# Optimization experiments

Hardware: AMD Instinct MI355X
Metric: run time of the kernel (lower is better)

The kernel has to match this reference:

```python
import jax, jax.numpy as jnp
import numpy as np

NUM_EMBEDDINGS = 8192
EMBEDDING_DIM = 256
COMMITMENT_COST = 0.25


def setup_inputs() -> dict:
    key = jax.random.key(0)
    k1, k2 = jax.random.split(key)
    z_e = jax.random.normal(k1, (32, EMBEDDING_DIM, 32, 32), dtype=jnp.float32)
    # nn.init.uniform_(weight, -1/K, 1/K)
    bound = 1.0 / NUM_EMBEDDINGS
    emb_w = jax.random.uniform(k2, (NUM_EMBEDDINGS, EMBEDDING_DIM), dtype=jnp.float32,
                               minval=-bound, maxval=bound)
    return {"z_e": z_e, "emb_w": emb_w}


def reference(z_e, emb_w):
    b, c, h, w = z_e.shape
    orig_dtype = z_e.dtype
    z = z_e.astype(jnp.float32)
    emb = emb_w.astype(jnp.float32)
    # [B,C,H,W] -> [N, C]
    z_flat = z.transpose(0, 2, 3, 1).reshape(-1, c)
    distances = (jnp.sum(z_flat * z_flat, axis=1, keepdims=True)
                 - 2.0 * (z_flat @ emb.T)
                 + jnp.sum(emb * emb, axis=1))
    encoding_indices = jnp.argmin(distances, axis=1)  # [N]
    z_q = emb[encoding_indices].reshape(b, h, w, c).transpose(0, 3, 1, 2)
    # eval path: commitment = cc * mse(stop_grad(z_e), z_q); codebook = mse(...)
    mse = jnp.mean((jax.lax.stop_gradient(z) - z_q) ** 2)
    vq_loss = (1.0 + COMMITMENT_COST) * mse
    # straight-through estimator
    z_q_st = (z + jax.lax.stop_gradient(z_q - z)).astype(orig_dtype)
    # perplexity from code usage histogram
    n_tokens = encoding_indices.shape[0]
    counts = jnp.zeros((NUM_EMBEDDINGS,), jnp.float32).at[encoding_indices].add(1.0)
    avg_probs = counts / n_tokens
    perplexity = jnp.exp(-jnp.sum(avg_probs * jnp.log(jnp.clip(avg_probs, 1e-10, None))))
    indices = encoding_indices.reshape(b, h, w)
    return z_q_st, vq_loss, perplexity, indices
```

## Files before the change

kernel.cpp:

```cpp
#include <hip/hip_runtime.h>
#include <hip/hip_fp16.h>
#include <cmath>
#include <float.h>

#define NUM_EMB 8192
#define DIM 256
#define HW 1024
#define N_TOK 32768
#define KSPLIT 2
#define KRANGE (NUM_EMB/KSPLIT)
#define OUT_ZQ_ELEMS 8388608

#define CAP 48
#define MARGIN_GP 0.4f

#define BM 128
#define BCODES 64
#define NBUF (KRANGE/BCODES)

#define WS_MSE    0
#define WS_COUNTS 64
#define WS_CNT    (WS_COUNTS + NUM_EMB*4)
#define WS_MEMSET_END (WS_CNT + KSPLIT*N_TOK*4)
#define WS_Z2     WS_MEMSET_END
#define WS_CANDI  (WS_Z2 + N_TOK*4)

typedef _Float16 half8 __attribute__((ext_vector_type(8)));
typedef _Float16 half4v __attribute__((ext_vector_type(4)));
typedef float f32x16 __attribute__((ext_vector_type(16)));
typedef __attribute__((address_space(3))) void lds_void;
typedef __attribute__((address_space(1))) const void gbl_void;

__global__ __launch_bounds__(256) void vq_pack_z(
    const float* __restrict__ z, _Float16* __restrict__ zh, float* __restrict__ z2)
{
    __shared__ float zt[32][257];
    __shared__ float rr[32][16];
    int t = threadIdx.x;
    int n0 = blockIdx.x * 32;
    int b = n0 >> 10, hw0 = n0 & 1023;
    const float* zb = z + (size_t)b * DIM * HW + hw0;
    int tn = t & 31, tc = t >> 5;
    #pragma unroll 4
    for (int it = 0; it < 32; it++) {
        int c = it * 8 + tc;
        zt[tn][c] = zb[(size_t)c * HW + tn];
    }
    __syncthreads();
    int tn2 = t & 31, tj = t >> 5;
    #pragma unroll
    for (int h = 0; h < 2; h++) {
        float v0 = zt[tn2][h*128 + tj];
        float r = __fmul_rn(v0, v0);
        for (int i = 8; i < 128; i += 8) {
            float v = zt[tn2][h*128 + i + tj];
            r = __fadd_rn(r, __fmul_rn(v, v));
        }
        rr[tn2][h*8 + tj] = r;
    }
    int row = t >> 3, seg = t & 7;
    half8 outv[4];
    #pragma unroll
    for (int q = 0; q < 4; q++)
        #pragma unroll
        for (int u = 0; u < 8; u++)
            outv[q][u] = (_Float16)zt[row][seg*32 + q*8 + u];
    half8* dst = (half8*)(zh + (size_t)(n0 + row) * DIM + seg * 32);
    #pragma unroll
    for (int q = 0; q < 4; q++) dst[q] = outv[q];
    __syncthreads();
    if (t < 32) {
        const float* rw = rr[t];
        float h0 = __fadd_rn(__fadd_rn(__fadd_rn(rw[0], rw[1]), __fadd_rn(rw[2], rw[3])),
                             __fadd_rn(__fadd_rn(rw[4], rw[5]), __fadd_rn(rw[6], rw[7])));
        float h1 = __fadd_rn(__fadd_rn(__fadd_rn(rw[8], rw[9]), __fadd_rn(rw[10], rw[11])),
                             __fadd_rn(__fadd_rn(rw[12], rw[13]), __fadd_rn(rw[14], rw[15])));
        z2[n0 + t] = __fadd_rn(h0, h1);
    }
}

__global__ __launch_bounds__(256) void vq_pack_e(
    const float* __restrict__ emb, _Float16* __restrict__ eh)
{
    int i = blockIdx.x * 256 + threadIdx.x;
    float4 v = ((const float4*)emb)[i];
    half4v h;
    h[0] = (_Float16)(v.x * 8192.0f);
    h[1] = (_Float16)(v.y * 8192.0f);
    h[2] = (_Float16)(v.z * 8192.0f);
    h[3] = (_Float16)(v.w * 8192.0f);
    *(half4v*)(eh + (size_t)i * 4) = h;
}

__global__ __launch_bounds__(512) void vq_dist_kernel(
    const _Float16* __restrict__ zh, const _Float16* __restrict__ eh,
    int* __restrict__ cnt, unsigned short* __restrict__ candi)
{
    __shared__ _Float16 Bs[2][16384];
    __shared__ float mx[2][BM];
    __shared__ int cntL[BM];
    int t = threadIdx.x;
    int w = t >> 6, lane = t & 63;
    int lm = lane & 31, lh = lane >> 5;
    int r = w >> 1, c = w & 1;
    int n0 = blockIdx.x * BM;
    int ks = blockIdx.y;
    int kbase = ks * KRANGE;

    if (t < BM) {
        cntL[t] = 0;
        mx[0][t] = -1e30f;
        mx[1][t] = -1e30f;
    }

    const _Float16* arow = zh + (size_t)(n0 + r*32 + lm) * DIM + lh * 8;
    half8 A[16];
    #pragma unroll
    for (int s = 0; s < 16; s++)
        A[s] = *(const half8*)(arow + s * 16);

    auto STAGE = [&](int ii, int b) {
        int cb0 = kbase + ii * BCODES;
        #pragma unroll
        for (int rr = 0; rr < 4; rr++) {
            int p = rr * 512 + t;
            int cd = p >> 5;
            int oc = ((p & 31) - cd) & 31;
            __builtin_amdgcn_global_load_lds(
                (gbl_void*)(eh + (size_t)(cb0 + cd) * DIM + oc * 8),
                (lds_void*)((char*)&Bs[b][0] + p * 16), 16, 0, 0);
        }
    };

    float m[16];
    #pragma unroll
    for (int e = 0; e < 16; e++) m[e] = -1e30f;

    int cl = c * 32 + lm;

    auto COMPUTE = [&](int i, int b) {
        {
            const float4* mb = (const float4*)&mx[c ^ 1][r * 32 + 4 * lh];
            #pragma unroll
            for (int g = 0; g < 4; g++) {
                float4 v = mb[2 * g];
                m[4*g+0] = fmaxf(m[4*g+0], v.x);
                m[4*g+1] = fmaxf(m[4*g+1], v.y);
                m[4*g+2] = fmaxf(m[4*g+2], v.z);
                m[4*g+3] = fmaxf(m[4*g+3], v.w);
            }
        }

        const _Float16* Bb = &Bs[b][0] + (size_t)cl * 256;
        f32x16 acc;
        #pragma unroll
        for (int e = 0; e < 16; e++) acc[e] = 0.f;

        __builtin_amdgcn_s_setprio(1);
        #pragma unroll
        for (int s = 0; s < 16; s++) {
            half8 bf = *(const half8*)(Bb + (((s*2 + lh) + cl) & 31) * 8);
            acc = __builtin_amdgcn_mfma_f32_32x32x16_f16(A[s], bf, acc, 0, 0, 0);
        }
        __builtin_amdgcn_s_setprio(0);

        #pragma unroll
        for (int e = 0; e < 16; e++) m[e] = fmaxf(m[e], acc[e]);
        bool doRed = (i < 4) || ((i & 3) == 3);
        if (doRed) {
            #pragma unroll
            for (int e = 0; e < 16; e++) {
                float q = m[e];
                #pragma unroll
                for (int o = 1; o <= 16; o <<= 1) q = fmaxf(q, __shfl_xor(q, o));
                m[e] = q;
            }
            if (lm == 0) {
                float4* mb = (float4*)&mx[c][r * 32 + 4 * lh];
                #pragma unroll
                for (int g = 0; g < 4; g++) {
                    float4 v = { m[4*g+0], m[4*g+1], m[4*g+2], m[4*g+3] };
                    mb[2 * g] = v;
                }
            }
        }
        int cb = kbase + i * BCODES;
        #pragma unroll
        for (int e = 0; e < 16; e++) {
            if (acc[e] > m[e] - MARGIN_GP) {
                int rowe = (e & 3) + 8 * (e >> 2) + 4 * lh;
                int tok = r * 32 + rowe;
                int slot = atomicAdd(&cntL[tok], 1);
                if (slot < CAP)
                    candi[((size_t)ks * N_TOK + n0 + tok) * CAP + slot] =
                        (unsigned short)(cb + cl);
            }
        }
    };

    STAGE(0, 0);
    for (int i = 0; i < NBUF; i += 2) {
        __syncthreads();
        STAGE(i + 1, 1);
        COMPUTE(i, 0);
        __syncthreads();
        if (i + 2 < NBUF) STAGE(i + 2, 0);
        COMPUTE(i + 1, 1);
    }

    __syncthreads();
    if (t < BM) cnt[ks * N_TOK + n0 + t] = cntL[t];
}

#define GT 32
__global__ __launch_bounds__(256) void vq_rg_kernel(
    const float* __restrict__ z, const float* __restrict__ emb,
    const float* __restrict__ z2, const int* __restrict__ cnt,
    const unsigned short* __restrict__ candi,
    int* __restrict__ counts, double* __restrict__ mse_sum,
    float* __restrict__ out_zq, float* __restrict__ out_idx)
{
    __shared__ float zs[GT][257];
    __shared__ float zq[GT][DIM];
    __shared__ unsigned long long kmin[GT];
    __shared__ int sidx[GT];
    __shared__ double red[4];
    int t = threadIdx.x;
    int n0 = blockIdx.x * GT;
    int b = n0 >> 10, hw0 = n0 & 1023;
    int lane = t & 63, w = t >> 6;

    {
        int nn = t & 31, cg = t >> 5;
        const float* zb = z + (size_t)b * DIM * HW + hw0 + nn;
        #pragma unroll 4
        for (int i = 0; i < 32; i++) {
            int c = i*8 + cg;
            zs[nn][c] = zb[(size_t)c * HW];
        }
    }
    if (t < GT) kmin[t] = ~0ULL;
    __syncthreads();

    int tcs0[8], po[9];
    int ovf8 = 0;
    po[0] = 0;
    #pragma unroll
    for (int i = 0; i < 8; i++) {
        int n = n0 + w*8 + i;
        int c0 = cnt[n], c1 = cnt[N_TOK + n];
        if (c0 > CAP || c1 > CAP) { c0 = 0; c1 = 0; ovf8 |= (1 << i); }
        tcs0[i] = c0;
        po[i+1] = po[i] + c0 + c1;
    }
    int total = po[8];

    for (int base = 0; base < total; base += 64) {
        int g = base + lane;
        unsigned long long key = ~0ULL;
        int mytok = -1;
        if (g < total) {
            int i = 0;
            #pragma unroll
            for (int q = 1; q < 8; q++) i += (g >= po[q]);
            int sl = g - po[i];
            int n = n0 + w*8 + i;
            int s = sl >= tcs0[i];
            int slot = s ? sl - tcs0[i] : sl;
            int code = candi[((size_t)s * N_TOK + n) * CAP + slot];
            int tok = w*8 + i;
            float accv = 0.f;
            const float4* ep = (const float4*)(emb + (size_t)code * DIM);
            #pragma unroll 8
            for (int q4 = 0; q4 < 64; q4++) {
                float4 e4 = ep[q4];
                accv = fmaf(zs[tok][q4*4+0], e4.x, accv);
                accv = fmaf(zs[tok][q4*4+1], e4.y, accv);
                accv = fmaf(zs[tok][q4*4+2], e4.z, accv);
                accv = fmaf(zs[tok][q4*4+3], e4.w, accv);
            }
            float d = fmaf(-2.f, accv, z2[n]);
            key = ((unsigned long long)__float_as_uint(d) << 32) | (unsigned)code;
            mytok = tok;
        }
        #pragma unroll
        for (int i = 0; i < 8; i++) {
            unsigned long long kk = (mytok == w*8 + i) ? key : ~0ULL;
            #pragma unroll
            for (int o = 32; o > 0; o >>= 1) {
                unsigned long long ob = __shfl_xor(kk, o);
                if (ob < kk) kk = ob;
            }
            if (lane == 0 && kk < kmin[w*8 + i]) kmin[w*8 + i] = kk;
        }
    }

    for (int i = 0; i < 8; i++) if (ovf8 & (1 << i)) {
        int tok = w*8 + i, n = n0 + tok;
        float z2n = z2[n];
        unsigned long long bst = ~0ULL;
        for (int k = lane; k < NUM_EMB; k += 64) {
            float accv = 0.f;
            const float4* ep = (const float4*)(emb + (size_t)k * DIM);
            #pragma unroll 8
            for (int q4 = 0; q4 < 64; q4++) {
                float4 e4 = ep[q4];
                accv = fmaf(zs[tok][q4*4+0], e4.x, accv);
                accv = fmaf(zs[tok][q4*4+1], e4.y, accv);
                accv = fmaf(zs[tok][q4*4+2], e4.z, accv);
                accv = fmaf(zs[tok][q4*4+3], e4.w, accv);
            }
            float d = fmaf(-2.f, accv, z2n);
            unsigned long long kk =
                ((unsigned long long)__float_as_uint(d) << 32) | (unsigned)k;
            if (kk < bst) bst = kk;
        }
        #pragma unroll
        for (int o = 32; o > 0; o >>= 1) {
            unsigned long long ob = __shfl_xor(bst, o);
            if (ob < bst) bst = ob;
        }
        if (lane == 0 && bst < kmin[tok]) kmin[tok] = bst;
    }
    __syncthreads();

    if (t < GT) {
        int bi = (int)(kmin[t] & 0xffffffffu);
        sidx[t] = bi;
        out_idx[n0 + t] = (float)bi;
        atomicAdd(&counts[bi], 1);
    }
    __syncthreads();

    for (int m = w*8; m < w*8 + 8; m++) {
        int row = sidx[m];
        float4 v = *(const float4*)(emb + (size_t)row * DIM + lane * 4);
        int cb = (lane + m) & 63;
        *(float4*)&zq[m][cb * 4] = v;
    }
    __syncthreads();

    int nn = t & 31, cc = t >> 5;
    float* op = out_zq + (size_t)b * DIM * HW + hw0 + nn;
    float lsum = 0.f;
    #pragma unroll 4
    for (int i = 0; i < 32; i++) {
        int c = i*8 + cc;
        int cb = ((c >> 2) + nn) & 63;
        float q = zq[nn][cb*4 + (c & 3)];
        float zv = zs[nn][c];
        op[(size_t)c * HW] = __fadd_rn(zv, __fsub_rn(q, zv));
        float d = zv - q;
        lsum = fmaf(d, d, lsum);
    }
    double ds = (double)lsum;
    #pragma unroll
    for (int off = 32; off > 0; off >>= 1)
        ds += __shfl_down(ds, off);
    if (lane == 0) red[w] = ds;
    __syncthreads();
    if (t == 0) atomicAdd(mse_sum, red[0] + red[1] + red[2] + red[3]);
}

__global__ __launch_bounds__(256) void vq_finalize_kernel(
    const double* __restrict__ mse_sum, const int* __restrict__ counts,
    float* __restrict__ out_scalars)
{
    __shared__ float red[4];
    int t = threadIdx.x;
    float local = 0.f;
    for (int k = t; k < NUM_EMB; k += 256) {
        int c = counts[k];
        if (c > 0) {
            float p = (float)c * (1.0f / (float)N_TOK);
            local += p * logf(p);
        }
    }
    int lane = t & 63, w = t >> 6;
    #pragma unroll
    for (int off = 32; off > 0; off >>= 1)
        local += __shfl_down(local, off);
    if (lane == 0) red[w] = local;
    __syncthreads();
    if (t == 0) {
        float s = red[0] + red[1] + red[2] + red[3];
        out_scalars[0] = 1.25f * (float)(*mse_sum * (1.0 / (double)OUT_ZQ_ELEMS));
        out_scalars[1] = expf(-s);
    }
}

extern "C" void kernel_launch(void* const* d_in, const int* in_sizes, int n_in,
                              void* d_out, int out_size, void* d_ws, size_t ws_size,
                              hipStream_t stream)
{
    const float* z   = (const float*)d_in[0];
    const float* emb = (const float*)d_in[1];
    float* out = (float*)d_out;
    char* ws = (char*)d_ws;
    double* mse_sum = (double*)(ws + WS_MSE);
    int*    counts  = (int*)(ws + WS_COUNTS);
    int*    cnt     = (int*)(ws + WS_CNT);
    float*  z2      = (float*)(ws + WS_Z2);
    unsigned short* candi = (unsigned short*)(ws + WS_CANDI);

    _Float16* zh = (_Float16*)d_out;
    _Float16* eh = (_Float16*)(out + 4194304);

    hipMemsetAsync(d_ws, 0, WS_MEMSET_END, stream);

    vq_pack_e<<<NUM_EMB*DIM/4/256, 256, 0, stream>>>(emb, eh);
    vq_pack_z<<<N_TOK/32, 256, 0, stream>>>(z, zh, z2);
    vq_dist_kernel<<<dim3(N_TOK/BM, KSPLIT), 512, 0, stream>>>(zh, eh, cnt, candi);
    vq_rg_kernel<<<N_TOK/GT, 256, 0, stream>>>(z, emb, z2, cnt, candi,
                                               counts, mse_sum,
                                               out, out + OUT_ZQ_ELEMS + 2);
    vq_finalize_kernel<<<1, 256, 0, stream>>>(mse_sum, counts, out + OUT_ZQ_ELEMS);
}
```

Baseline: 472.2 us.

## Split codebook four ways and drop cross-wave max sharing in distance kernel

The distance kernel now splits the codebook into four K-ranges instead of two and uses 256-thread blocks. Each wave covers all 32 codes of a smaller 32-code tile, so the LDS exchange of running maxima between paired waves is removed. The per-split candidate cap drops to 24, and the rescoring kernel now merges candidates from four splits. The aim is more blocks in flight, less LDS and cross-wave synchronisation, and smaller tiles. In exchange, each split's running max is less tight, so more candidates are emitted and the overflow fallback triggers more often. Candidate rescoring work also grows.

```diff
diff --git a/kernel.cpp b/kernel.cpp
--- a/kernel.cpp
+++ b/kernel.cpp
@@ -7,15 +7,15 @@
 #define DIM 256
 #define HW 1024
 #define N_TOK 32768
-#define KSPLIT 2
+#define KSPLIT 4
 #define KRANGE (NUM_EMB/KSPLIT)
 #define OUT_ZQ_ELEMS 8388608
 
-#define CAP 48
+#define CAP 24
 #define MARGIN_GP 0.4f
 
 #define BM 128
-#define BCODES 64
+#define BCODES 32
 #define NBUF (KRANGE/BCODES)
 
 #define WS_MSE    0
@@ -92,28 +92,22 @@
     *(half4v*)(eh + (size_t)i * 4) = h;
 }
 
-__global__ __launch_bounds__(512) void vq_dist_kernel(
+__global__ __launch_bounds__(256) void vq_dist_kernel(
     const _Float16* __restrict__ zh, const _Float16* __restrict__ eh,
     int* __restrict__ cnt, unsigned short* __restrict__ candi)
 {
-    __shared__ _Float16 Bs[2][16384];
-    __shared__ float mx[2][BM];
+    __shared__ _Float16 Bs[2][8192];
     __shared__ int cntL[BM];
     int t = threadIdx.x;
     int w = t >> 6, lane = t & 63;
     int lm = lane & 31, lh = lane >> 5;
-    int r = w >> 1, c = w & 1;
     int n0 = blockIdx.x * BM;
     int ks = blockIdx.y;
     int kbase = ks * KRANGE;
 
-    if (t < BM) {
-        cntL[t] = 0;
-        mx[0][t] = -1e30f;
-        mx[1][t] = -1e30f;
-    }
-
-    const _Float16* arow = zh + (size_t)(n0 + r*32 + lm) * DIM + lh * 8;
+    if (t < BM) cntL[t] = 0;
+
+    const _Float16* arow = zh + (size_t)(n0 + w*32 + lm) * DIM + lh * 8;
     half8 A[16];
     #pragma unroll
     for (int s = 0; s < 16; s++)
@@ -123,7 +117,7 @@
         int cb0 = kbase + ii * BCODES;
         #pragma unroll
         for (int rr = 0; rr < 4; rr++) {
-            int p = rr * 512 + t;
+            int p = rr * 256 + t;
             int cd = p >> 5;
             int oc = ((p & 31) - cd) & 31;
             __builtin_amdgcn_global_load_lds(
@@ -136,21 +130,10 @@
     #pragma unroll
     for (int e = 0; e < 16; e++) m[e] = -1e30f;
 
-    int cl = c * 32 + lm;
+    int cl = lm;
+    int tloc = w * 32 + 4 * lh;
 
     auto COMPUTE = [&](int i, int b) {
-        {
-            const float4* mb = (const float4*)&mx[c ^ 1][r * 32 + 4 * lh];
-            #pragma unroll
-            for (int g = 0; g < 4; g++) {
-                float4 v = mb[2 * g];
-                m[4*g+0] = fmaxf(m[4*g+0], v.x);
-                m[4*g+1] = fmaxf(m[4*g+1], v.y);
-                m[4*g+2] = fmaxf(m[4*g+2], v.z);
-                m[4*g+3] = fmaxf(m[4*g+3], v.w);
-            }
-        }
-
         const _Float16* Bb = &Bs[b][0] + (size_t)cl * 256;
         f32x16 acc;
         #pragma unroll
@@ -175,21 +158,12 @@
                 for (int o = 1; o <= 16; o <<= 1) q = fmaxf(q, __shfl_xor(q, o));
                 m[e] = q;
             }
-            if (lm == 0) {
-                float4* mb = (float4*)&mx[c][r * 32 + 4 * lh];
-                #pragma unroll
-                for (int g = 0; g < 4; g++) {
-                    float4 v = { m[4*g+0], m[4*g+1], m[4*g+2], m[4*g+3] };
-                    mb[2 * g] = v;
-                }
-            }
         }
         int cb = kbase + i * BCODES;
         #pragma unroll
         for (int e = 0; e < 16; e++) {
             if (acc[e] > m[e] - MARGIN_GP) {
-                int rowe = (e & 3) + 8 * (e >> 2) + 4 * lh;
-                int tok = r * 32 + rowe;
+                int tok = tloc + (e & 3) + 8 * (e >> 2);
                 int slot = atomicAdd(&cntL[tok], 1);
                 if (slot < CAP)
                     candi[((size_t)ks * N_TOK + n0 + tok) * CAP + slot] =
@@ -242,16 +216,21 @@
     if (t < GT) kmin[t] = ~0ULL;
     __syncthreads();
 
-    int tcs0[8], po[9];
+    int tb1[8], tb2[8], tb3[8], po[9];
     int ovf8 = 0;
     po[0] = 0;
     #pragma unroll
     for (int i = 0; i < 8; i++) {
         int n = n0 + w*8 + i;
-        int c0 = cnt[n], c1 = cnt[N_TOK + n];
-        if (c0 > CAP || c1 > CAP) { c0 = 0; c1 = 0; ovf8 |= (1 << i); }
-        tcs0[i] = c0;
-        po[i+1] = po[i] + c0 + c1;
+        int c0 = cnt[n],             c1 = cnt[N_TOK + n];
+        int c2 = cnt[2*N_TOK + n],   c3 = cnt[3*N_TOK + n];
+        if (c0 > CAP || c1 > CAP || c2 > CAP || c3 > CAP) {
+            c0 = c1 = c2 = c3 = 0; ovf8 |= (1 << i);
+        }
+        tb1[i] = c0;
+        tb2[i] = c0 + c1;
+        tb3[i] = c0 + c1 + c2;
+        po[i+1] = po[i] + c0 + c1 + c2 + c3;
     }
     int total = po[8];
 
@@ -265,8 +244,11 @@
             for (int q = 1; q < 8; q++) i += (g >= po[q]);
             int sl = g - po[i];
             int n = n0 + w*8 + i;
-            int s = sl >= tcs0[i];
-            int slot = s ? sl - tcs0[i] : sl;
+            int s = 0, off = 0;
+            if (sl >= tb1[i]) { s = 1; off = tb1[i]; }
+            if (sl >= tb2[i]) { s = 2; off = tb2[i]; }
+            if (sl >= tb3[i]) { s = 3; off = tb3[i]; }
+            int slot = sl - off;
             int code = candi[((size_t)s * N_TOK + n) * CAP + slot];
             int tok = w*8 + i;
             float accv = 0.f;
@@ -410,7 +392,7 @@
 
     vq_pack_e<<<NUM_EMB*DIM/4/256, 256, 0, stream>>>(emb, eh);
     vq_pack_z<<<N_TOK/32, 256, 0, stream>>>(z, zh, z2);
-    vq_dist_kernel<<<dim3(N_TOK/BM, KSPLIT), 512, 0, stream>>>(zh, eh, cnt, candi);
+    vq_dist_kernel<<<dim3(N_TOK/BM, KSPLIT), 256, 0, stream>>>(zh, eh, cnt, candi);
     vq_rg_kernel<<<N_TOK/GT, 256, 0, stream>>>(z, emb, z2, cnt, candi,
                                                counts, mse_sum,
                                                out, out + OUT_ZQ_ELEMS + 2);
```

Result: slower. 501.0 us (+6.1%).
